# Kernel optimization log

Measured on AMD Instinct MI355X. Metric: run time of the kernel, lower is better.

Reference implementation:

```python
import jax, jax.numpy as jnp
import numpy as np

B, C, N, HID = 1, 64, 1024, 128


def setup_inputs() -> dict:
    key = jax.random.key(0)
    k1, k2, k3, k4, k5 = jax.random.split(key, 5)
    x = jax.random.normal(k1, (B, C, N), dtype=jnp.float32)
    # Conv2d(2C -> HID, 1): weight [HID, 2C] (1x1 kernel flattened), bias [HID]
    W1 = jax.random.normal(k2, (HID, 2 * C), dtype=jnp.float32) * (1.0 / np.sqrt(2 * C))
    b1 = jax.random.normal(k3, (HID,), dtype=jnp.float32) * 0.01
    # Conv2d(HID -> 1, 1): weight [HID], bias [1]
    W2 = jax.random.normal(k4, (HID,), dtype=jnp.float32) * (1.0 / np.sqrt(HID))
    b2 = jax.random.normal(k5, (1,), dtype=jnp.float32) * 0.01
    return {"x": x, "W1": W1, "b1": b1, "W2": W2, "b2": b2}


def reference(x, W1, b1, W2, b2):
    # Original: m1[b,c,i,j] = x[b,c,j]; m2[b,c,i,j] = x[b,c,i]; block = cat([m1, m2], dim=1)
    # tanh is elementwise, and the 1x1 conv is linear, so we split W1 into the
    # halves acting on m1 (j-indexed) and m2 (i-indexed) and avoid the explicit
    # O(N^2 * 2C) repeat+concat. The nonlinear hidden tensor [B,HID,N,N] is the
    # same math as Conv2d(tanh(block)).
    c = x.shape[1]
    t = jnp.tanh(x)                                   # [B, C, N]
    pj = jnp.einsum('hc,bcn->bhn', W1[:, :c], t)      # contribution of m1 (varies over j)
    pi = jnp.einsum('hc,bcn->bhn', W1[:, c:], t)      # contribution of m2 (varies over i)
    h = jnp.tanh(pi[:, :, :, None] + pj[:, :, None, :] + b1[None, :, None, None])  # [B,HID,N,N]
    e = jnp.einsum('h,bhij->bij', W2, h) + b2[0]      # [B, N, N]
    return e + jnp.swapaxes(e, 1, 2)
```

## Files before the change

kernel.cpp:

```cpp
#include <hip/hip_runtime.h>
#include <math.h>

#define CN  64
#define NN  1024
#define HIDN 128

__global__ __launch_bounds__(256) void prep_kernel(
    const float* __restrict__ x, const float* __restrict__ W1,
    const float* __restrict__ b1, const float* __restrict__ W2,
    float4* __restrict__ S)
{
    __shared__ float t_s[8][68];
    const int tid = threadIdx.x;
    const int n0  = blockIdx.x * 8;

    for (int idx = tid; idx < 8 * CN; idx += 256) {
        int nl = idx & 7, c = idx >> 3;
        t_s[nl][c] = tanhf(x[c * NN + n0 + nl]);
    }
    __syncthreads();

    const int nl = tid & 7;
    int h = tid >> 3;
    for (int k = 0; k < 4; ++k, h += 32) {
        const float4* wrow = (const float4*)(W1 + h * (2 * CN));
        float pj = 0.f, pi = 0.f;
#pragma unroll
        for (int c4 = 0; c4 < 16; ++c4) {
            float4 tv = *(const float4*)&t_s[nl][c4 * 4];
            float4 wl = wrow[c4];
            float4 wh = wrow[16 + c4];
            pj = fmaf(wl.x, tv.x, fmaf(wl.y, tv.y, fmaf(wl.z, tv.z, fmaf(wl.w, tv.w, pj))));
            pi = fmaf(wh.x, tv.x, fmaf(wh.y, tv.y, fmaf(wh.z, tv.z, fmaf(wh.w, tv.w, pi))));
        }
        float U  = tanhf(pi + b1[h]);
        float V  = tanhf(pj);
        float w2 = W2[h];
        S[h * NN + n0 + nl] = make_float4(U, w2 * U, V, w2 * V);
    }
}

__device__ __forceinline__ void sym_term(const float4& A, const float4& B, float& acc)
{
    float d1 = fmaf(A.x, B.z, 1.0f);
    float d2 = fmaf(B.x, A.z, 1.0f);
    float n1 = A.y + B.w;
    float n2 = B.y + A.w;
    float r  = __builtin_amdgcn_rcpf(d1 * d2);
    acc = fmaf(n1, d2 * r, fmaf(n2, d1 * r, acc));
}

__global__ __launch_bounds__(256) void pair_kernel(
    const float4* __restrict__ S, const float* __restrict__ b2,
    float* __restrict__ out)
{
    const int bj = blockIdx.x, bi = blockIdx.y;
    if (bi > bj) return;

    __shared__ float4 Si[32][32];
    __shared__ float4 Sj[32][32];

    const int tid = threadIdx.x;
    const int tx = tid & 15, ty = tid >> 4;
    const int i0 = bi * 32, j0 = bj * 32;

    float acc00 = 0.f, acc01 = 0.f, acc10 = 0.f, acc11 = 0.f;

    for (int hc = 0; hc < 4; ++hc) {
        const int h0 = hc * 32;
        __syncthreads();
#pragma unroll
        for (int k = 0; k < 4; ++k) {
            int t  = tid + k * 256;
            int hl = t >> 5, nl = t & 31;
            Si[hl][nl] = S[(h0 + hl) * NN + i0 + nl];
            Sj[hl][nl] = S[(h0 + hl) * NN + j0 + nl];
        }
        __syncthreads();
#pragma unroll 8
        for (int hl = 0; hl < 32; ++hl) {
            float4 A0 = Si[hl][ty];
            float4 A1 = Si[hl][ty + 16];
            float4 B0 = Sj[hl][tx];
            float4 B1 = Sj[hl][tx + 16];
            sym_term(A0, B0, acc00);
            sym_term(A0, B1, acc01);
            sym_term(A1, B0, acc10);
            sym_term(A1, B1, acc11);
        }
    }

    const float bias2 = 2.0f * b2[0];
    const float v00 = acc00 + bias2, v01 = acc01 + bias2;
    const float v10 = acc10 + bias2, v11 = acc11 + bias2;

    out[(i0 + ty)      * NN + j0 + tx]      = v00;
    out[(i0 + ty)      * NN + j0 + tx + 16] = v01;
    out[(i0 + ty + 16) * NN + j0 + tx]      = v10;
    out[(i0 + ty + 16) * NN + j0 + tx + 16] = v11;

    if (bi != bj) {
        __syncthreads();
        float* T = (float*)&Si[0][0];
        T[ty * 33 + tx]             = v00;
        T[ty * 33 + tx + 16]        = v01;
        T[(ty + 16) * 33 + tx]      = v10;
        T[(ty + 16) * 33 + tx + 16] = v11;
        __syncthreads();
        out[(j0 + ty)      * NN + i0 + tx]      = T[tx * 33 + ty];
        out[(j0 + ty)      * NN + i0 + tx + 16] = T[(tx + 16) * 33 + ty];
        out[(j0 + ty + 16) * NN + i0 + tx]      = T[tx * 33 + ty + 16];
        out[(j0 + ty + 16) * NN + i0 + tx + 16] = T[(tx + 16) * 33 + ty + 16];
    }
}

extern "C" void kernel_launch(void* const* d_in, const int* in_sizes, int n_in,
                              void* d_out, int out_size, void* d_ws, size_t ws_size,
                              hipStream_t stream)
{
    const float* x  = (const float*)d_in[0];
    const float* W1 = (const float*)d_in[1];
    const float* b1 = (const float*)d_in[2];
    const float* W2 = (const float*)d_in[3];
    const float* b2 = (const float*)d_in[4];
    float* out = (float*)d_out;
    float4* S  = (float4*)d_ws;

    prep_kernel<<<128, 256, 0, stream>>>(x, W1, b1, W2, S);
    pair_kernel<<<dim3(32, 32), 256, 0, stream>>>(S, b2, out);
}
```

Measured before the change: 112.2 us.

## Split hidden dimension across blocks, shrink S to float2, add combine kernel

The pair kernel now launches a compact triangular grid instead of a 32x32 grid with early exits. Off-diagonal tiles split the 128 hidden units into two halves run by separate blocks, written to the upper and lower tiles, and a new combine kernel sums them and adds the bias. S shrinks from float4 to float2, with W2 applied inside the pair loop. The prep kernel switches to an exp-based fast tanh with more blocks, and the pair term is algebraically reduced to one fused numerator. This targets load imbalance and tail underutilisation, at the cost of an extra launch, an extra read/write pass over the output, and some loss of tanh accuracy.

```diff
diff --git a/kernel.cpp b/kernel.cpp
--- a/kernel.cpp
+++ b/kernel.cpp
@@ -1,64 +1,92 @@
 #include <hip/hip_runtime.h>
 #include <math.h>
 
-#define CN  64
-#define NN  1024
+#define CN   64
+#define NN   1024
 #define HIDN 128
+#define NDIAG 528
+#define NOFF  496
+
+__device__ __forceinline__ float tanh_fast(float x) {
+    float e = __expf(2.0f * x);
+    return 1.0f - 2.0f * __builtin_amdgcn_rcpf(e + 1.0f);
+}
 
 __global__ __launch_bounds__(256) void prep_kernel(
     const float* __restrict__ x, const float* __restrict__ W1,
-    const float* __restrict__ b1, const float* __restrict__ W2,
-    float4* __restrict__ S)
-{
-    __shared__ float t_s[8][68];
+    const float* __restrict__ b1, float2* __restrict__ S)
+{
+    __shared__ float t_s[2][64];
     const int tid = threadIdx.x;
-    const int n0  = blockIdx.x * 8;
-
-    for (int idx = tid; idx < 8 * CN; idx += 256) {
-        int nl = idx & 7, c = idx >> 3;
-        t_s[nl][c] = tanhf(x[c * NN + n0 + nl]);
+    const int n0  = blockIdx.x * 2;
+
+    if (tid < 64) {
+        float2 xv = *(const float2*)&x[tid * NN + n0];
+        t_s[0][tid] = tanh_fast(xv.x);
+        t_s[1][tid] = tanh_fast(xv.y);
     }
     __syncthreads();
 
-    const int nl = tid & 7;
-    int h = tid >> 3;
-    for (int k = 0; k < 4; ++k, h += 32) {
-        const float4* wrow = (const float4*)(W1 + h * (2 * CN));
-        float pj = 0.f, pi = 0.f;
-#pragma unroll
-        for (int c4 = 0; c4 < 16; ++c4) {
-            float4 tv = *(const float4*)&t_s[nl][c4 * 4];
-            float4 wl = wrow[c4];
-            float4 wh = wrow[16 + c4];
-            pj = fmaf(wl.x, tv.x, fmaf(wl.y, tv.y, fmaf(wl.z, tv.z, fmaf(wl.w, tv.w, pj))));
-            pi = fmaf(wh.x, tv.x, fmaf(wh.y, tv.y, fmaf(wh.z, tv.z, fmaf(wh.w, tv.w, pi))));
-        }
-        float U  = tanhf(pi + b1[h]);
-        float V  = tanhf(pj);
-        float w2 = W2[h];
-        S[h * NN + n0 + nl] = make_float4(U, w2 * U, V, w2 * V);
-    }
-}
-
-__device__ __forceinline__ void sym_term(const float4& A, const float4& B, float& acc)
-{
-    float d1 = fmaf(A.x, B.z, 1.0f);
-    float d2 = fmaf(B.x, A.z, 1.0f);
-    float n1 = A.y + B.w;
-    float n2 = B.y + A.w;
+    const int h  = tid & 127;
+    const int nl = tid >> 7;
+    const float4* wrow = (const float4*)(W1 + h * (2 * CN));
+
+    float pj[4] = {0.f, 0.f, 0.f, 0.f};
+    float pi[4] = {0.f, 0.f, 0.f, 0.f};
+#pragma unroll
+    for (int c4 = 0; c4 < 16; ++c4) {
+        float4 tv = *(const float4*)&t_s[nl][c4 * 4];
+        float4 wl = wrow[c4];
+        float4 wh = wrow[16 + c4];
+        const int s = c4 & 3;
+        pj[s] = fmaf(wl.x, tv.x, fmaf(wl.y, tv.y, fmaf(wl.z, tv.z, fmaf(wl.w, tv.w, pj[s]))));
+        pi[s] = fmaf(wh.x, tv.x, fmaf(wh.y, tv.y, fmaf(wh.z, tv.z, fmaf(wh.w, tv.w, pi[s]))));
+    }
+    float pjs = (pj[0] + pj[1]) + (pj[2] + pj[3]);
+    float pis = (pi[0] + pi[1]) + (pi[2] + pi[3]);
+    float U = tanh_fast(pis + b1[h]);
+    float V = tanh_fast(pjs);
+    S[h * NN + n0 + nl] = make_float2(U, V);
+}
+
+__device__ __forceinline__ void sym_term(float w2h, float2 A, float2 B, float& acc)
+{
+    float d1 = fmaf(A.x, B.y, 1.0f);
+    float d2 = fmaf(B.x, A.y, 1.0f);
+    float n1 = A.x + B.y;
+    float n2 = B.x + A.y;
     float r  = __builtin_amdgcn_rcpf(d1 * d2);
-    acc = fmaf(n1, d2 * r, fmaf(n2, d1 * r, acc));
+    float t  = fmaf(n1, d2, n2 * d1);
+    acc = fmaf(w2h, t * r, acc);
 }
 
 __global__ __launch_bounds__(256) void pair_kernel(
-    const float4* __restrict__ S, const float* __restrict__ b2,
-    float* __restrict__ out)
-{
-    const int bj = blockIdx.x, bi = blockIdx.y;
-    if (bi > bj) return;
-
-    __shared__ float4 Si[32][32];
-    __shared__ float4 Sj[32][32];
+    const float2* __restrict__ S, const float* __restrict__ W2,
+    const float* __restrict__ b2, float* __restrict__ out)
+{
+    const int id = blockIdx.x;
+    int bi, bj, h0, nchunk;
+    bool chunk1;
+    if (id < NDIAG) {
+        int t = id;
+        int r = (int)((sqrtf(8.f * t + 1.f) - 1.f) * 0.5f);
+        while ((r + 1) * (r + 2) / 2 <= t) ++r;
+        while (r * (r + 1) / 2 > t) --r;
+        int c = t - r * (r + 1) / 2;
+        bi = c; bj = r; chunk1 = false;
+        h0 = 0; nchunk = (bi == bj) ? 4 : 2;
+    } else {
+        int t = id - NDIAG;
+        int r = (int)((1.f + sqrtf(8.f * t + 1.f)) * 0.5f);
+        while (r * (r - 1) / 2 > t) --r;
+        while (r * (r + 1) / 2 <= t) ++r;
+        int c = t - r * (r - 1) / 2;
+        bi = c; bj = r; chunk1 = true;
+        h0 = 64; nchunk = 2;
+    }
+
+    __shared__ float2 Si[32][32];
+    __shared__ float2 Sj[32][32];
 
     const int tid = threadIdx.x;
     const int tx = tid & 15, ty = tid >> 4;
@@ -66,51 +94,93 @@
 
     float acc00 = 0.f, acc01 = 0.f, acc10 = 0.f, acc11 = 0.f;
 
-    for (int hc = 0; hc < 4; ++hc) {
-        const int h0 = hc * 32;
+    for (int hc = 0; hc < nchunk; ++hc) {
+        const int hbase = h0 + hc * 32;
         __syncthreads();
 #pragma unroll
         for (int k = 0; k < 4; ++k) {
-            int t  = tid + k * 256;
-            int hl = t >> 5, nl = t & 31;
-            Si[hl][nl] = S[(h0 + hl) * NN + i0 + nl];
-            Sj[hl][nl] = S[(h0 + hl) * NN + j0 + nl];
+            int t2 = tid + k * 256;
+            int hl = t2 >> 5, nl = t2 & 31;
+            Si[hl][nl] = S[(hbase + hl) * NN + i0 + nl];
+            Sj[hl][nl] = S[(hbase + hl) * NN + j0 + nl];
         }
         __syncthreads();
 #pragma unroll 8
         for (int hl = 0; hl < 32; ++hl) {
-            float4 A0 = Si[hl][ty];
-            float4 A1 = Si[hl][ty + 16];
-            float4 B0 = Sj[hl][tx];
-            float4 B1 = Sj[hl][tx + 16];
-            sym_term(A0, B0, acc00);
-            sym_term(A0, B1, acc01);
-            sym_term(A1, B0, acc10);
-            sym_term(A1, B1, acc11);
+            float w2h = W2[hbase + hl];
+            float2 A0 = Si[hl][ty];
+            float2 A1 = Si[hl][ty + 16];
+            float2 B0 = Sj[hl][tx];
+            float2 B1 = Sj[hl][tx + 16];
+            sym_term(w2h, A0, B0, acc00);
+            sym_term(w2h, A0, B1, acc01);
+            sym_term(w2h, A1, B0, acc10);
+            sym_term(w2h, A1, B1, acc11);
         }
     }
 
-    const float bias2 = 2.0f * b2[0];
-    const float v00 = acc00 + bias2, v01 = acc01 + bias2;
-    const float v10 = acc10 + bias2, v11 = acc11 + bias2;
-
-    out[(i0 + ty)      * NN + j0 + tx]      = v00;
-    out[(i0 + ty)      * NN + j0 + tx + 16] = v01;
-    out[(i0 + ty + 16) * NN + j0 + tx]      = v10;
-    out[(i0 + ty + 16) * NN + j0 + tx + 16] = v11;
-
-    if (bi != bj) {
+    if (!chunk1) {
+        float v00 = acc00, v01 = acc01, v10 = acc10, v11 = acc11;
+        if (bi == bj) {
+            const float bias2 = 2.0f * b2[0];
+            v00 += bias2; v01 += bias2; v10 += bias2; v11 += bias2;
+        }
+        out[(i0 + ty)      * NN + j0 + tx]      = v00;
+        out[(i0 + ty)      * NN + j0 + tx + 16] = v01;
+        out[(i0 + ty + 16) * NN + j0 + tx]      = v10;
+        out[(i0 + ty + 16) * NN + j0 + tx + 16] = v11;
+    } else {
         __syncthreads();
         float* T = (float*)&Si[0][0];
-        T[ty * 33 + tx]             = v00;
-        T[ty * 33 + tx + 16]        = v01;
-        T[(ty + 16) * 33 + tx]      = v10;
-        T[(ty + 16) * 33 + tx + 16] = v11;
+        T[ty * 33 + tx]             = acc00;
+        T[ty * 33 + tx + 16]        = acc01;
+        T[(ty + 16) * 33 + tx]      = acc10;
+        T[(ty + 16) * 33 + tx + 16] = acc11;
         __syncthreads();
         out[(j0 + ty)      * NN + i0 + tx]      = T[tx * 33 + ty];
         out[(j0 + ty)      * NN + i0 + tx + 16] = T[(tx + 16) * 33 + ty];
         out[(j0 + ty + 16) * NN + i0 + tx]      = T[tx * 33 + ty + 16];
         out[(j0 + ty + 16) * NN + i0 + tx + 16] = T[(tx + 16) * 33 + ty + 16];
+    }
+}
+
+__global__ __launch_bounds__(256) void combine_kernel(
+    const float* __restrict__ b2, float* __restrict__ out)
+{
+    int t = blockIdx.x;
+    int r = (int)((1.f + sqrtf(8.f * t + 1.f)) * 0.5f);
+    while (r * (r - 1) / 2 > t) --r;
+    while (r * (r + 1) / 2 <= t) ++r;
+    int c = t - r * (r - 1) / 2;
+    const int i0 = c * 32, j0 = r * 32;
+
+    __shared__ float Ua[32][33];
+    __shared__ float Lb[32][33];
+    const int tid = threadIdx.x;
+    const int tx = tid & 15, ty = tid >> 4;
+
+    Ua[ty][tx]           = out[(i0 + ty)      * NN + j0 + tx];
+    Ua[ty][tx + 16]      = out[(i0 + ty)      * NN + j0 + tx + 16];
+    Ua[ty + 16][tx]      = out[(i0 + ty + 16) * NN + j0 + tx];
+    Ua[ty + 16][tx + 16] = out[(i0 + ty + 16) * NN + j0 + tx + 16];
+    Lb[ty][tx]           = out[(j0 + ty)      * NN + i0 + tx];
+    Lb[ty][tx + 16]      = out[(j0 + ty)      * NN + i0 + tx + 16];
+    Lb[ty + 16][tx]      = out[(j0 + ty + 16) * NN + i0 + tx];
+    Lb[ty + 16][tx + 16] = out[(j0 + ty + 16) * NN + i0 + tx + 16];
+    __syncthreads();
+
+    const float bias2 = 2.0f * b2[0];
+#pragma unroll
+    for (int k = 0; k < 4; ++k) {
+        int ry = ty + (k >> 1) * 16;
+        int cx = tx + (k & 1) * 16;
+        out[(i0 + ry) * NN + j0 + cx] = Ua[ry][cx] + Lb[cx][ry] + bias2;
+    }
+#pragma unroll
+    for (int k = 0; k < 4; ++k) {
+        int ry = ty + (k >> 1) * 16;
+        int cx = tx + (k & 1) * 16;
+        out[(j0 + ry) * NN + i0 + cx] = Ua[cx][ry] + Lb[ry][cx] + bias2;
     }
 }
 
@@ -124,8 +194,9 @@
     const float* W2 = (const float*)d_in[3];
     const float* b2 = (const float*)d_in[4];
     float* out = (float*)d_out;
-    float4* S  = (float4*)d_ws;
-
-    prep_kernel<<<128, 256, 0, stream>>>(x, W1, b1, W2, S);
-    pair_kernel<<<dim3(32, 32), 256, 0, stream>>>(S, b2, out);
-}
+    float2* S  = (float2*)d_ws;
+
+    prep_kernel<<<512, 256, 0, stream>>>(x, W1, b1, S);
+    pair_kernel<<<NDIAG + NOFF, 256, 0, stream>>>(S, W2, b2, out);
+    combine_kernel<<<NOFF, 256, 0, stream>>>(b2, out);
+}
```

Measured after the change: 98.91 us. 11.9% less time.
